# Optimization experiments

Measured on AMD Instinct MI355X. Metric: run time of the kernel, lower is better.

Reference implementation:

```python
import jax, jax.numpy as jnp
import numpy as np

N = 50000      # nodes
E = 800000     # edges
IN = 128       # input feature dim
H = 4          # attention heads
D = 32         # per-head hidden dim
L = 3          # GAT layers
C = 32         # num classes
SLOPE = 0.2    # leaky relu negative slope


def _glorot(key, shape):
    fan_in, fan_out = shape[0], shape[-1]
    std = np.sqrt(2.0 / (fan_in + fan_out))
    return jax.random.normal(key, shape, dtype=jnp.float32) * std


def setup_inputs() -> dict:
    key = jax.random.key(0)
    ks = jax.random.split(key, 16)
    inp = {
        "x": jax.random.normal(ks[0], (N, IN), dtype=jnp.float32),
        "src": jax.random.randint(ks[1], (E,), 0, N, dtype=jnp.int32),
        "dst": jax.random.randint(ks[2], (E,), 0, N, dtype=jnp.int32),
        # layer 0: in_dim -> H*D
        "W0": _glorot(ks[3], (IN, H * D)),
        "al0": _glorot(ks[4], (H, D)),
        "ar0": _glorot(ks[5], (H, D)),
        # layers 1,2: H*D -> H*D
        "W1": _glorot(ks[6], (H * D, H * D)),
        "al1": _glorot(ks[7], (H, D)),
        "ar1": _glorot(ks[8], (H, D)),
        "W2": _glorot(ks[9], (H * D, H * D)),
        "al2": _glorot(ks[10], (H, D)),
        "ar2": _glorot(ks[11], (H, D)),
        # JK concat projection: L*H*D -> C (bias=False)
        "Wproj": _glorot(ks[12], (L * H * D, C)),
    }
    return inp


def gat_layer(h, W, al, ar, src, dst):
    """DGL-style GATConv (no residual, no dropout), ELU activation."""
    feat = (h @ W).reshape(N, H, D)                      # [N,H,D]
    el = jnp.sum(feat * al, axis=-1)                     # [N,H]
    er = jnp.sum(feat * ar, axis=-1)                     # [N,H]
    e = jax.nn.leaky_relu(el[src] + er[dst], negative_slope=SLOPE)  # [E,H]
    # edge softmax over incoming edges per destination node
    m = jax.lax.stop_gradient(jax.ops.segment_max(e, dst, num_segments=N))
    ex = jnp.exp(e - m[dst])                             # [E,H]
    s = jax.ops.segment_sum(ex, dst, num_segments=N)     # [N,H]
    a = ex / s[dst]                                      # [E,H]
    out = jax.ops.segment_sum(feat[src] * a[:, :, None], dst, num_segments=N)
    return jax.nn.elu(out).reshape(N, H * D)             # flatten(1)


def reference(x, src, dst, W0, al0, ar0, W1, al1, ar1, W2, al2, ar2, Wproj):
    h0 = gat_layer(x, W0, al0, ar0, src, dst)
    h1 = gat_layer(h0, W1, al1, ar1, src, dst)
    h2 = gat_layer(h1, W2, al2, ar2, src, dst)
    emb = jnp.concatenate([h0, h1, h2], axis=1)          # [N, L*H*D]
    logits = emb @ Wproj                                 # [N, C]
    return logits
```

## Files before the change

kernel.cpp:

```cpp
#include <hip/hip_runtime.h>
#include <hip/hip_fp16.h>
#include <math.h>

#define NNODES 50000
#define NEDGES 800000
#define HD     128
#define NHEADS 4
#define DH     32

#define TILE_R 64
#define AKPF   136

#define NBUCK  196
#define BCAP   6144
#define P1_T   512
#define P1_EPB 4096
#define P2_T   512

struct alignas(16) Half8 { __half2 a, b, c, d; };
typedef _Float16 f16x8 __attribute__((ext_vector_type(8)));
typedef float    f32x4 __attribute__((ext_vector_type(4)));
typedef float    f32x8 __attribute__((ext_vector_type(8)));

static __device__ __forceinline__ float lrelu(float x){ return x > 0.f ? x : 0.2f*x; }
static __device__ __forceinline__ float elu(float x){ return x > 0.f ? x : __expf(x) - 1.f; }

__global__ void prep_kernel(const float* __restrict__ W0, const float* __restrict__ W1,
                            const float* __restrict__ W2, const float* __restrict__ Wp,
                            _Float16* __restrict__ wt, _Float16* __restrict__ wt2,
                            int* __restrict__ btail){
  int id = blockIdx.x*blockDim.x + threadIdx.x;
  if (id < NBUCK) btail[id] = id*BCAP;
  if (id < 3*16384){
    int l = id >> 14, rem = id & 16383;
    int n = rem >> 7, k = rem & 127;
    const float* W = (l==0) ? W0 : (l==1) ? W1 : W2;
    wt[(size_t)l*16384 + n*128 + k] = (_Float16)W[k*128 + n];
  } else if (id < 3*16384 + 12288){
    int rem = id - 3*16384;
    int k = rem >> 5, n = rem & 31;
    wt2[n*384 + k] = (_Float16)Wp[k*32 + n];
  }
}


__global__ __launch_bounds__(P1_T) void p1_bucket_kernel(
    const int* __restrict__ src, const int* __restrict__ dst,
    int* __restrict__ btail, unsigned int* __restrict__ bstage, int e)
{
  __shared__ int cnt[NBUCK];
  __shared__ int gstart[NBUCK];
  int t = threadIdx.x;
  int base = blockIdx.x * P1_EPB;
  for (int i = t; i < NBUCK; i += P1_T) cnt[i] = 0;
  __syncthreads();
  int s_[8], b_[8], dl_[8];
  #pragma unroll
  for (int j = 0; j < 8; j++){
    int i = base + j*P1_T + t;
    if (i < e){
      int d = dst[i];
      s_[j]  = src[i];
      b_[j]  = d >> 8;
      dl_[j] = d & 255;
      atomicAdd(&cnt[b_[j]], 1);
    } else b_[j] = -1;
  }
  __syncthreads();
  for (int i = t; i < NBUCK; i += P1_T){
    gstart[i] = cnt[i] ? atomicAdd(&btail[i], cnt[i]) : 0;
    cnt[i] = 0;
  }
  __syncthreads();
  #pragma unroll
  for (int j = 0; j < 8; j++){
    if (b_[j] >= 0){
      int p = atomicAdd(&cnt[b_[j]], 1);
      bstage[(size_t)gstart[b_[j]] + p] = ((unsigned)dl_[j] << 16) | (unsigned)s_[j];
    }
  }
}

__global__ __launch_bounds__(256) void bucket_scan_kernel(
    const int* __restrict__ btail, int* __restrict__ ebase, int* __restrict__ rowptr)
{
  __shared__ int c[256];
  int t = threadIdx.x;
  int mine = (t < NBUCK) ? (btail[t] - t*BCAP) : 0;
  c[t] = mine;
  __syncthreads();
  for (int off = 1; off < 256; off <<= 1){
    int v = 0;
    if (t >= off) v = c[t - off];
    __syncthreads();
    c[t] += v;
    __syncthreads();
  }
  if (t < NBUCK) ebase[t] = c[t] - mine;
  if (t == NBUCK - 1) rowptr[NNODES] = c[t];
}

__global__ __launch_bounds__(P2_T) void p2_csr_kernel(
    const unsigned int* __restrict__ bstage, const int* __restrict__ btail,
    const int* __restrict__ ebase, int* __restrict__ rowptr, int* __restrict__ srcs)
{
  __shared__ unsigned int ebuf[BCAP];
  __shared__ unsigned short sorted[BCAP];
  __shared__ int cnt[256], ofs[256], run[256];
  int b = blockIdx.x, t = threadIdx.x;
  int nE = btail[b] - b*BCAP;
  int gb = ebase[b];
  const unsigned int* bp = bstage + (size_t)b*BCAP;

  for (int i = t; i < 256; i += P2_T) cnt[i] = 0;
  __syncthreads();
  for (int i = t; i < nE; i += P2_T){
    unsigned int v = bp[i];
    ebuf[i] = v;
    atomicAdd(&cnt[v >> 16], 1);
  }
  __syncthreads();
  if (t < 256) ofs[t] = cnt[t];
  __syncthreads();
  for (int off = 1; off < 256; off <<= 1){
    int v = 0;
    if (t < 256 && t >= off) v = ofs[t - off];
    __syncthreads();
    if (t < 256) ofs[t] += v;
    __syncthreads();
  }
  if (t < 256){
    int ex = ofs[t] - cnt[t];
    run[t] = ex;
    int node = b*256 + t;
    if (node < NNODES) rowptr[node] = gb + ex;
  }
  __syncthreads();
  for (int i = t; i < nE; i += P2_T){
    unsigned int v = ebuf[i];
    int p = atomicAdd(&run[v >> 16], 1);
    sorted[p] = (unsigned short)(v & 0xFFFFu);
  }
  __syncthreads();
  for (int i = t; i < nE; i += P2_T)
    srcs[gb + i] = (int)sorted[i];
}

template<bool FP16IN>
__global__ __launch_bounds__(256) void gemm_feat_kernel(
    const void* __restrict__ hin, int hstride,
    const _Float16* __restrict__ Wt,
    const float* __restrict__ al, const float* __restrict__ ar,
    __half* __restrict__ feat, float* __restrict__ elv, float* __restrict__ erv)
{
  __shared__ __align__(16) _Float16 Ah[TILE_R*AKPF];
  __shared__ __align__(16) _Float16 Wh[HD*AKPF];
  int t = threadIdx.x;
  int w = t >> 6, lane = t & 63;
  int c = lane & 15, quad = lane >> 4;
  int rbase = blockIdx.x * TILE_R;

  f32x4 acc[8];
  #pragma unroll
  for (int ct = 0; ct < 8; ct++) acc[ct] = (f32x4){0.f, 0.f, 0.f, 0.f};

  int arow = t >> 2;
  int akq  = t & 3;
  int an   = rbase + arow;
  if (FP16IN){
    const _Float16* ap = (const _Float16*)hin + (size_t)an*hstride + akq*8;
    #pragma unroll
    for (int kb = 0; kb < HD; kb += 32){
      f16x8 av = (f16x8)((_Float16)0);
      if (an < NNODES) av = *(const f16x8*)(ap + kb);
      *(f16x8*)&Ah[arow*AKPF + kb + akq*8] = av;
    }
  } else {
    const float* ap = (const float*)hin + (size_t)an*hstride + akq*8;
    #pragma unroll
    for (int kb = 0; kb < HD; kb += 32){
      float4 v0 = make_float4(0.f,0.f,0.f,0.f), v1 = v0;
      if (an < NNODES){
        v0 = *(const float4*)(ap + kb);
        v1 = *(const float4*)(ap + kb + 4);
      }
      f16x8 av;
      av[0]=(_Float16)v0.x; av[1]=(_Float16)v0.y; av[2]=(_Float16)v0.z; av[3]=(_Float16)v0.w;
      av[4]=(_Float16)v1.x; av[5]=(_Float16)v1.y; av[6]=(_Float16)v1.z; av[7]=(_Float16)v1.w;
      *(f16x8*)&Ah[arow*AKPF + kb + akq*8] = av;
    }
  }
  int wn = t >> 1;
  int wk = (t & 1) * 16;
  const _Float16* wp = Wt + wn*HD + wk;
  #pragma unroll
  for (int kb = 0; kb < HD; kb += 32){
    *(uint4*)&Wh[wn*AKPF + kb + wk]     = *(const uint4*)(wp + kb);
    *(uint4*)&Wh[wn*AKPF + kb + wk + 8] = *(const uint4*)(wp + kb + 8);
  }
  __syncthreads();

  #pragma unroll
  for (int kb = 0; kb < HD; kb += 32){
    f16x8 afrag = *(const f16x8*)&Ah[(w*16 + c)*AKPF + kb + quad*8];
    #pragma unroll
    for (int ct = 0; ct < 8; ct++){
      f16x8 bfrag = *(const f16x8*)&Wh[(ct*16 + c)*AKPF + kb + quad*8];
      acc[ct] = __builtin_amdgcn_mfma_f32_16x16x32_f16(afrag, bfrag, acc[ct], 0, 0, 0);
    }
  }

  float alv[8], arv[8];
  #pragma unroll
  for (int ct = 0; ct < 8; ct++){
    int idx = (ct >> 1)*DH + (ct & 1)*16 + c;
    alv[ct] = al[idx];
    arv[ct] = ar[idx];
  }
  #pragma unroll
  for (int r = 0; r < 4; r++){
    int n = rbase + w*16 + quad*4 + r;
    float pl[4], pr[4];
    #pragma unroll
    for (int hh = 0; hh < 4; hh++){
      pl[hh] = acc[2*hh][r]*alv[2*hh] + acc[2*hh+1][r]*alv[2*hh+1];
      pr[hh] = acc[2*hh][r]*arv[2*hh] + acc[2*hh+1][r]*arv[2*hh+1];
    }
    #pragma unroll
    for (int hh = 0; hh < 4; hh++){
      pl[hh] += __shfl_xor(pl[hh], 1); pl[hh] += __shfl_xor(pl[hh], 2);
      pl[hh] += __shfl_xor(pl[hh], 4); pl[hh] += __shfl_xor(pl[hh], 8);
      pr[hh] += __shfl_xor(pr[hh], 1); pr[hh] += __shfl_xor(pr[hh], 2);
      pr[hh] += __shfl_xor(pr[hh], 4); pr[hh] += __shfl_xor(pr[hh], 8);
    }
    if (n < NNODES){
      if (c < 4){ elv[n*NHEADS + c] = pl[c]; erv[n*NHEADS + c] = pr[c]; }
      #pragma unroll
      for (int ct = 0; ct < 8; ct++)
        feat[(size_t)n*HD + ct*16 + c] = __float2half_rn(acc[ct][r]);
    }
  }
}

#define MIX2(alo, ahi, pk, aa) \
  asm("v_fma_mix_f32 %0, %2, %3, %0 op_sel:[0,0,0] op_sel_hi:[1,0,0]\n\t" \
      "v_fma_mix_f32 %1, %2, %3, %1 op_sel:[1,0,0] op_sel_hi:[1,0,0]" \
      : "+v"(alo), "+v"(ahi) : "v"(pk), "v"(aa))

__global__ __launch_bounds__(256) void smax_agg_kernel(
    const int* __restrict__ rowptr, const int* __restrict__ srcs,
    const float* __restrict__ elv, const float* __restrict__ erv,
    const __half* __restrict__ feat, __half* __restrict__ emb_out, int n)
{
  int gid = (int)((blockIdx.x*(size_t)blockDim.x + threadIdx.x) >> 3);
  if (gid >= n) return;
  int fl8  = threadIdx.x & 7;
  int fo   = fl8 * 16;
  int head = fl8 >> 1;

  int s0 = rowptr[gid], s1 = rowptr[gid+1];
  float erh = erv[gid*4 + head];

  float acc[16];
  #pragma unroll
  for (int j = 0; j < 16; j++) acc[j] = 0.f;
  float ssum = 0.f;

  const uint4 zq = make_uint4(0,0,0,0);

  int   sA[4], sB[4];
  uint4 qA0[4], qA1[4], qB0[4], qB1[4];
  float eA[4], eB[4];

#define LOADB(base, S, Q0, Q1, EL)                                   \
  {                                                                  \
    _Pragma("unroll")                                                \
    for (int j = 0; j < 4; j++){                                     \
      int ee = (base) + j;                                           \
      S[j] = (ee < s1) ? srcs[ee] : -1;                              \
    }                                                                \
    _Pragma("unroll")                                                \
    for (int j = 0; j < 4; j++){                                     \
      if (S[j] >= 0){                                                \
        const __half* fr = feat + ((size_t)S[j] << 7) + fo;          \
        Q0[j] = *(const uint4*)(fr);                                 \
        Q1[j] = *(const uint4*)(fr + 8);                             \
        EL[j] = elv[S[j]*4 + head];                                  \
      } else { Q0[j] = zq; Q1[j] = zq; EL[j] = 0.f; }                \
    }                                                                \
  }

#define ACCB(S, Q0, Q1, EL)                                          \
  {                                                                  \
    _Pragma("unroll")                                                \
    for (int j = 0; j < 4; j++){                                     \
      float x = EL[j] + erh;                                         \
      float a = (S[j] >= 0) ? __expf(fmaxf(x, 0.2f*x)) : 0.f;        \
      ssum += a;                                                     \
      MIX2(acc[0],  acc[1],  Q0[j].x, a);                            \
      MIX2(acc[2],  acc[3],  Q0[j].y, a);                            \
      MIX2(acc[4],  acc[5],  Q0[j].z, a);                            \
      MIX2(acc[6],  acc[7],  Q0[j].w, a);                            \
      MIX2(acc[8],  acc[9],  Q1[j].x, a);                            \
      MIX2(acc[10], acc[11], Q1[j].y, a);                            \
      MIX2(acc[12], acc[13], Q1[j].z, a);                            \
      MIX2(acc[14], acc[15], Q1[j].w, a);                            \
    }                                                                \
  }

  LOADB(s0, sA, qA0, qA1, eA);
  for (int e = s0; e < s1; e += 8){
    LOADB(e + 4, sB, qB0, qB1, eB);
    ACCB(sA, qA0, qA1, eA);
    LOADB(e + 8, sA, qA0, qA1, eA);
    ACCB(sB, qB0, qB1, eB);
  }
#undef LOADB
#undef ACCB

  float inv = (ssum > 0.f) ? 1.f / ssum : 0.f;
  __half2 hv[8];
  #pragma unroll
  for (int j = 0; j < 8; j++)
    hv[j] = __floats2half2_rn(elu(acc[2*j]*inv), elu(acc[2*j+1]*inv));
  __half* op = emb_out + (size_t)gid*384 + fo;
  *(uint4*)(op)     = *(uint4*)&hv[0];
  *(uint4*)(op + 8) = *(uint4*)&hv[4];
}

__global__ __launch_bounds__(256) void proj_mfma_kernel(
    const __half* __restrict__ emb, const _Float16* __restrict__ Wt2,
    float* __restrict__ out)
{
  __shared__ __align__(16) _Float16 Ah[128*136];
  __shared__ __align__(16) _Float16 Bh[32*392];
  int t = threadIdx.x;
  int w = t >> 6, lane = t & 63;
  int c = lane & 15, quad = lane >> 4;
  int rbase = blockIdx.x * 128;

  f32x4 acc[2][2];
  #pragma unroll
  for (int rt = 0; rt < 2; rt++)
    #pragma unroll
    for (int ct = 0; ct < 2; ct++) acc[rt][ct] = (f32x4){0.f,0.f,0.f,0.f};

  #pragma unroll
  for (int i = 0; i < 6; i++){
    int idx = i*256 + t;
    int row = idx / 48;
    int q8  = idx - row*48;
    *(f16x8*)&Bh[row*392 + q8*8] = *(const f16x8*)(Wt2 + row*384 + q8*8);
  }

  for (int kc = 0; kc < 384; kc += 128){
    #pragma unroll
    for (int i = 0; i < 8; i++){
      int idx = i*256 + t;
      int row = idx >> 4;
      int q   = idx & 15;
      int gr  = rbase + row;
      f16x8 v = (f16x8)((_Float16)0);
      if (gr < NNODES) v = *(const f16x8*)((const _Float16*)emb + (size_t)gr*384 + kc + q*8);
      *(f16x8*)&Ah[row*136 + q*8] = v;
    }
    __syncthreads();
    #pragma unroll
    for (int kb = 0; kb < 128; kb += 32){
      #pragma unroll
      for (int rt = 0; rt < 2; rt++){
        f16x8 afrag = *(const f16x8*)&Ah[(w*32 + rt*16 + c)*136 + kb + quad*8];
        #pragma unroll
        for (int ct = 0; ct < 2; ct++){
          f16x8 bfrag = *(const f16x8*)&Bh[(ct*16 + c)*392 + kc + kb + quad*8];
          acc[rt][ct] = __builtin_amdgcn_mfma_f32_16x16x32_f16(afrag, bfrag, acc[rt][ct], 0, 0, 0);
        }
      }
    }
    __syncthreads();
  }

  #pragma unroll
  for (int rt = 0; rt < 2; rt++)
    #pragma unroll
    for (int r = 0; r < 4; r++){
      int n = rbase + w*32 + rt*16 + quad*4 + r;
      if (n < NNODES){
        out[(size_t)n*32 + c]      = acc[rt][0][r];
        out[(size_t)n*32 + 16 + c] = acc[rt][1][r];
      }
    }
}

extern "C" void kernel_launch(void* const* d_in, const int* in_sizes, int n_in,
                              void* d_out, int out_size, void* d_ws, size_t ws_size,
                              hipStream_t stream) {
  const float* x    = (const float*)d_in[0];
  const int*   src  = (const int*)d_in[1];
  const int*   dst  = (const int*)d_in[2];
  const float* Ws_[3]  = { (const float*)d_in[3], (const float*)d_in[6], (const float*)d_in[9]  };
  const float* als[3] = { (const float*)d_in[4], (const float*)d_in[7], (const float*)d_in[10] };
  const float* ars[3] = { (const float*)d_in[5], (const float*)d_in[8], (const float*)d_in[11] };
  const float* Wproj  = (const float*)d_in[12];
  float* out = (float*)d_out;

  char* wptr = (char*)d_ws;
  auto alloc = [&](size_t bytes) -> void* {
    void* p = (void*)wptr; wptr += (bytes + 255) & ~(size_t)255; return p;
  };
  int*      btail      = (int*)     alloc((size_t)NBUCK*4);
  int*      ebase      = (int*)     alloc((size_t)NBUCK*4);
  unsigned* bstage     = (unsigned*)alloc((size_t)NBUCK*BCAP*4);
  int*      rowptr     = (int*)     alloc((size_t)(NNODES+1)*4);
  int*      src_sorted = (int*)     alloc((size_t)NEDGES*4);
  __half*   feat       = (__half*)  alloc((size_t)NNODES*HD*2);
  float*    elv        = (float*)   alloc((size_t)NNODES*NHEADS*4);
  float*    erv        = (float*)   alloc((size_t)NNODES*NHEADS*4);
  __half*   emb        = (__half*)  alloc((size_t)NNODES*384*2);
  _Float16* wt         = (_Float16*)alloc((size_t)3*HD*HD*2);
  _Float16* wt2        = (_Float16*)alloc((size_t)32*384*2);

  prep_kernel<<<(3*16384 + 12288 + 255)/256, 256, 0, stream>>>(
      Ws_[0], Ws_[1], Ws_[2], Wproj, wt, wt2, btail);

  p1_bucket_kernel<<<(NEDGES + P1_EPB - 1)/P1_EPB, P1_T, 0, stream>>>(
      src, dst, btail, bstage, NEDGES);
  bucket_scan_kernel<<<1, 256, 0, stream>>>(btail, ebase, rowptr);
  p2_csr_kernel<<<NBUCK, P2_T, 0, stream>>>(bstage, btail, ebase, rowptr, src_sorted);

  const int NGB = (NNODES + TILE_R - 1)/TILE_R;
  const int NSMB = (NNODES*8 + 255)/256;
  gemm_feat_kernel<false><<<NGB, 256, 0, stream>>>(
      (const void*)x, 128, wt, als[0], ars[0], feat, elv, erv);
  smax_agg_kernel<<<NSMB, 256, 0, stream>>>(rowptr, src_sorted, elv, erv,
                                            feat, emb, NNODES);
  for (int l = 1; l < 3; l++){
    gemm_feat_kernel<true><<<NGB, 256, 0, stream>>>(
        (const void*)(emb + (size_t)(l-1)*128), 384,
        wt + (size_t)l*HD*HD, als[l], ars[l], feat, elv, erv);
    smax_agg_kernel<<<NSMB, 256, 0, stream>>>(rowptr, src_sorted, elv, erv,
                                              feat, emb + (size_t)l*128, NNODES);
  }

  proj_mfma_kernel<<<(NNODES + 127)/128, 256, 0, stream>>>(emb, wt2, out);
}
```

Measured before the change: 273.1 us.

## Slice feature and embedding tensors by 16-column chunks for cache-local gathers

```diff
diff --git a/kernel.cpp b/kernel.cpp
--- a/kernel.cpp
+++ b/kernel.cpp
@@ -17,12 +17,11 @@
 #define P1_EPB 4096
 #define P2_T   512
 
-struct alignas(16) Half8 { __half2 a, b, c, d; };
+#define NCHUNK 196
+
 typedef _Float16 f16x8 __attribute__((ext_vector_type(8)));
 typedef float    f32x4 __attribute__((ext_vector_type(4)));
-typedef float    f32x8 __attribute__((ext_vector_type(8)));
-
-static __device__ __forceinline__ float lrelu(float x){ return x > 0.f ? x : 0.2f*x; }
+
 static __device__ __forceinline__ float elu(float x){ return x > 0.f ? x : __expf(x) - 1.f; }
 
 __global__ void prep_kernel(const float* __restrict__ W0, const float* __restrict__ W1,
@@ -81,39 +80,31 @@
   }
 }
 
-__global__ __launch_bounds__(256) void bucket_scan_kernel(
-    const int* __restrict__ btail, int* __restrict__ ebase, int* __restrict__ rowptr)
-{
-  __shared__ int c[256];
-  int t = threadIdx.x;
-  int mine = (t < NBUCK) ? (btail[t] - t*BCAP) : 0;
-  c[t] = mine;
-  __syncthreads();
-  for (int off = 1; off < 256; off <<= 1){
-    int v = 0;
-    if (t >= off) v = c[t - off];
-    __syncthreads();
-    c[t] += v;
-    __syncthreads();
-  }
-  if (t < NBUCK) ebase[t] = c[t] - mine;
-  if (t == NBUCK - 1) rowptr[NNODES] = c[t];
-}
-
 __global__ __launch_bounds__(P2_T) void p2_csr_kernel(
     const unsigned int* __restrict__ bstage, const int* __restrict__ btail,
-    const int* __restrict__ ebase, int* __restrict__ rowptr, int* __restrict__ srcs)
+    int* __restrict__ rowptr, int* __restrict__ srcs)
 {
   __shared__ unsigned int ebuf[BCAP];
   __shared__ unsigned short sorted[BCAP];
   __shared__ int cnt[256], ofs[256], run[256];
+  __shared__ int pf[256];
   int b = blockIdx.x, t = threadIdx.x;
+
+  if (t < 256) pf[t] = (t < NBUCK) ? (btail[t] - t*BCAP) : 0;
+  for (int i = t; i < 256; i += P2_T) cnt[i] = 0;
+  __syncthreads();
+  for (int off = 1; off < 256; off <<= 1){
+    int v = 0;
+    if (t < 256 && t >= off) v = pf[t - off];
+    __syncthreads();
+    if (t < 256) pf[t] += v;
+    __syncthreads();
+  }
   int nE = btail[b] - b*BCAP;
-  int gb = ebase[b];
+  int gb = pf[b] - nE;
+  if (b == 0 && t == 0) rowptr[NNODES] = pf[NBUCK-1];
   const unsigned int* bp = bstage + (size_t)b*BCAP;
 
-  for (int i = t; i < 256; i += P2_T) cnt[i] = 0;
-  __syncthreads();
   for (int i = t; i < nE; i += P2_T){
     unsigned int v = bp[i];
     ebuf[i] = v;
@@ -168,11 +159,13 @@
   int akq  = t & 3;
   int an   = rbase + arow;
   if (FP16IN){
-    const _Float16* ap = (const _Float16*)hin + (size_t)an*hstride + akq*8;
+    const _Float16* base = (const _Float16*)hin;
+    int off = (akq & 1) * 8;
     #pragma unroll
     for (int kb = 0; kb < HD; kb += 32){
+      int sl = (kb >> 4) + (akq >> 1);
       f16x8 av = (f16x8)((_Float16)0);
-      if (an < NNODES) av = *(const f16x8*)(ap + kb);
+      if (an < NNODES) av = *(const f16x8*)(base + (((size_t)sl*NNODES + an) << 4) + off);
       *(f16x8*)&Ah[arow*AKPF + kb + akq*8] = av;
     }
   } else {
@@ -237,7 +230,7 @@
       if (c < 4){ elv[n*NHEADS + c] = pl[c]; erv[n*NHEADS + c] = pr[c]; }
       #pragma unroll
       for (int ct = 0; ct < 8; ct++)
-        feat[(size_t)n*HD + ct*16 + c] = __float2half_rn(acc[ct][r]);
+        feat[((size_t)ct*NNODES + n)*16 + c] = __float2half_rn(acc[ct][r]);
     }
   }
 }
@@ -250,39 +243,41 @@
 __global__ __launch_bounds__(256) void smax_agg_kernel(
     const int* __restrict__ rowptr, const int* __restrict__ srcs,
     const float* __restrict__ elv, const float* __restrict__ erv,
-    const __half* __restrict__ feat, __half* __restrict__ emb_out, int n)
+    const __half* __restrict__ feat,
+    __half* __restrict__ emb_out,
+    int n)
 {
-  int gid = (int)((blockIdx.x*(size_t)blockDim.x + threadIdx.x) >> 3);
-  if (gid >= n) return;
-  int fl8  = threadIdx.x & 7;
-  int fo   = fl8 * 16;
-  int head = fl8 >> 1;
-
-  int s0 = rowptr[gid], s1 = rowptr[gid+1];
-  float erh = erv[gid*4 + head];
+  int bid  = blockIdx.x;
+  int s    = bid & 7;
+  int node = (bid >> 3)*256 + threadIdx.x;
+  if (node >= n) return;
+  int head = s >> 1;
+
+  int s0 = rowptr[node], s1 = rowptr[node+1];
+  float erh = erv[node*4 + head];
+  const __half* fbase = feat + (size_t)s*NNODES*16;
 
   float acc[16];
   #pragma unroll
   for (int j = 0; j < 16; j++) acc[j] = 0.f;
   float ssum = 0.f;
-
   const uint4 zq = make_uint4(0,0,0,0);
 
-  int   sA[4], sB[4];
-  uint4 qA0[4], qA1[4], qB0[4], qB1[4];
-  float eA[4], eB[4];
-
-#define LOADB(base, S, Q0, Q1, EL)                                   \
+  int   SA[2], SB[2];
+  uint4 A0[2], A1[2], B0[2], B1[2];
+  float EA[2], EB[2];
+
+#define LOADB(base_e, S, Q0, Q1, EL)                                 \
   {                                                                  \
     _Pragma("unroll")                                                \
-    for (int j = 0; j < 4; j++){                                     \
-      int ee = (base) + j;                                           \
+    for (int j = 0; j < 2; j++){                                     \
+      int ee = (base_e) + j;                                         \
       S[j] = (ee < s1) ? srcs[ee] : -1;                              \
     }                                                                \
     _Pragma("unroll")                                                \
-    for (int j = 0; j < 4; j++){                                     \
+    for (int j = 0; j < 2; j++){                                     \
       if (S[j] >= 0){                                                \
-        const __half* fr = feat + ((size_t)S[j] << 7) + fo;          \
+        const __half* fr = fbase + (size_t)S[j]*16;                  \
         Q0[j] = *(const uint4*)(fr);                                 \
         Q1[j] = *(const uint4*)(fr + 8);                             \
         EL[j] = elv[S[j]*4 + head];                                  \
@@ -293,7 +288,7 @@
 #define ACCB(S, Q0, Q1, EL)                                          \
   {                                                                  \
     _Pragma("unroll")                                                \
-    for (int j = 0; j < 4; j++){                                     \
+    for (int j = 0; j < 2; j++){                                     \
       float x = EL[j] + erh;                                         \
       float a = (S[j] >= 0) ? __expf(fmaxf(x, 0.2f*x)) : 0.f;        \
       ssum += a;                                                     \
@@ -308,12 +303,12 @@
     }                                                                \
   }
 
-  LOADB(s0, sA, qA0, qA1, eA);
-  for (int e = s0; e < s1; e += 8){
-    LOADB(e + 4, sB, qB0, qB1, eB);
-    ACCB(sA, qA0, qA1, eA);
-    LOADB(e + 8, sA, qA0, qA1, eA);
-    ACCB(sB, qB0, qB1, eB);
+  LOADB(s0, SA, A0, A1, EA);
+  for (int e = s0; e < s1; e += 4){
+    LOADB(e + 2, SB, B0, B1, EB);
+    ACCB(SA, A0, A1, EA);
+    LOADB(e + 4, SA, A0, A1, EA);
+    ACCB(SB, B0, B1, EB);
   }
 #undef LOADB
 #undef ACCB
@@ -323,7 +318,7 @@
   #pragma unroll
   for (int j = 0; j < 8; j++)
     hv[j] = __floats2half2_rn(elu(acc[2*j]*inv), elu(acc[2*j+1]*inv));
-  __half* op = emb_out + (size_t)gid*384 + fo;
+  __half* op = emb_out + ((size_t)s*NNODES + node)*16;
   *(uint4*)(op)     = *(uint4*)&hv[0];
   *(uint4*)(op + 8) = *(uint4*)&hv[4];
 }
@@ -360,8 +355,12 @@
       int row = idx >> 4;
       int q   = idx & 15;
       int gr  = rbase + row;
+      int pos = kc + q*8;
+      int ls  = pos >> 4;
+      int off = pos & 15;
       f16x8 v = (f16x8)((_Float16)0);
-      if (gr < NNODES) v = *(const f16x8*)((const _Float16*)emb + (size_t)gr*384 + kc + q*8);
+      if (gr < NNODES)
+        v = *(const f16x8*)((const _Float16*)emb + (((size_t)ls*NNODES + gr) << 4) + off);
       *(f16x8*)&Ah[row*136 + q*8] = v;
     }
     __syncthreads();
@@ -409,14 +408,13 @@
     void* p = (void*)wptr; wptr += (bytes + 255) & ~(size_t)255; return p;
   };
   int*      btail      = (int*)     alloc((size_t)NBUCK*4);
-  int*      ebase      = (int*)     alloc((size_t)NBUCK*4);
   unsigned* bstage     = (unsigned*)alloc((size_t)NBUCK*BCAP*4);
   int*      rowptr     = (int*)     alloc((size_t)(NNODES+1)*4);
   int*      src_sorted = (int*)     alloc((size_t)NEDGES*4);
-  __half*   feat       = (__half*)  alloc((size_t)NNODES*HD*2);
+  __half*   feat       = (__half*)  alloc((size_t)8*NNODES*16*2);
   float*    elv        = (float*)   alloc((size_t)NNODES*NHEADS*4);
   float*    erv        = (float*)   alloc((size_t)NNODES*NHEADS*4);
-  __half*   emb        = (__half*)  alloc((size_t)NNODES*384*2);
+  __half*   emb        = (__half*)  alloc((size_t)24*NNODES*16*2);
   _Float16* wt         = (_Float16*)alloc((size_t)3*HD*HD*2);
   _Float16* wt2        = (_Float16*)alloc((size_t)32*384*2);
 
@@ -425,21 +423,20 @@
 
   p1_bucket_kernel<<<(NEDGES + P1_EPB - 1)/P1_EPB, P1_T, 0, stream>>>(
       src, dst, btail, bstage, NEDGES);
-  bucket_scan_kernel<<<1, 256, 0, stream>>>(btail, ebase, rowptr);
-  p2_csr_kernel<<<NBUCK, P2_T, 0, stream>>>(bstage, btail, ebase, rowptr, src_sorted);
+  p2_csr_kernel<<<NBUCK, P2_T, 0, stream>>>(bstage, btail, rowptr, src_sorted);
 
   const int NGB = (NNODES + TILE_R - 1)/TILE_R;
-  const int NSMB = (NNODES*8 + 255)/256;
+  const int NSMB = NCHUNK * 8;
   gemm_feat_kernel<false><<<NGB, 256, 0, stream>>>(
       (const void*)x, 128, wt, als[0], ars[0], feat, elv, erv);
   smax_agg_kernel<<<NSMB, 256, 0, stream>>>(rowptr, src_sorted, elv, erv,
                                             feat, emb, NNODES);
   for (int l = 1; l < 3; l++){
     gemm_feat_kernel<true><<<NGB, 256, 0, stream>>>(
-        (const void*)(emb + (size_t)(l-1)*128), 384,
+        (const void*)(emb + (size_t)(l-1)*8*NNODES*16), 0,
         wt + (size_t)l*HD*HD, als[l], ars[l], feat, elv, erv);
     smax_agg_kernel<<<NSMB, 256, 0, stream>>>(rowptr, src_sorted, elv, erv,
-                                              feat, emb + (size_t)l*128, NNODES);
+                                              feat, emb + (size_t)l*8*NNODES*16, NNODES);
   }
 
   proj_mfma_kernel<<<(NNODES + 127)/128, 256, 0, stream>>>(emb, wt2, out);
```

Result: slower. 405.5 us (+48.5%).
